# Optimization experiments

Measured on AMD Instinct MI355X. Metric: run time of the kernel, lower is better.

## Reference

```python
import jax, jax.numpy as jnp
import numpy as np

B, S, D = 16, 4096, 1024
DIM_K, DIM_V, NUM_HEAD = 1024, 1024, 16


def setup_inputs() -> dict:
    key = jax.random.key(0)
    ks = jax.random.split(key, 7)
    s_in = 1.0 / np.sqrt(D)
    return {
        "x": jax.random.normal(ks[0], (B, S, D), dtype=jnp.float32),
        "Wq": jax.random.normal(ks[1], (D, DIM_K), dtype=jnp.float32) * s_in,
        "bq": jnp.zeros((DIM_K,), dtype=jnp.float32),
        "Wk": jax.random.normal(ks[2], (D, DIM_K), dtype=jnp.float32) * s_in,
        "bk": jnp.zeros((DIM_K,), dtype=jnp.float32),
        "Wv": jax.random.normal(ks[3], (D, DIM_V), dtype=jnp.float32) * s_in,
        "bv": jnp.zeros((DIM_V,), dtype=jnp.float32),
    }


def reference(x, Wq, bq, Wk, bk, Wv, bv):
    H = NUM_HEAD
    b, s, _ = x.shape
    Q = x @ Wq + bq                      # (B,S,dim_k)
    K = x @ Wk + bk                      # (B,S,dim_k)
    V = x @ Wv + bv                      # (B,S,dim_v)
    Q_ = Q.reshape(b, s, H, DIM_K // H)  # (B,S,H,dk)
    K_ = K.reshape(b, s, H, DIM_K // H)
    V_ = V.reshape(b, s, H, DIM_V // H)
    # NOTE: faithful to the source quirk — scores are across HEADS (H x H)
    # at each (batch, seq) position; no 1/sqrt(dim_k) scaling (unused in source).
    scores = jnp.einsum("bshd,bsgd->bshg", Q_, K_)   # (B,S,H,H)
    atten = jax.nn.softmax(scores, axis=-1)
    out = jnp.einsum("bshg,bsgd->bshd", atten, V_)    # (B,S,H,dv_head)
    return out.reshape(b, s, -1)                      # (B,S,dim_v)
```

## Files before the change

kernel.cpp:

```cpp
#include <hip/hip_runtime.h>
#include <stdint.h>

#define M_TOTAL 65536
#define DIM     1024
#define NQKV    3072
#define NHEAD   16
#define HDIM    64

typedef __attribute__((ext_vector_type(8))) _Float16 f16x8;
typedef __attribute__((ext_vector_type(4))) _Float16 f16x4;
typedef __attribute__((ext_vector_type(4))) float    f32x4;

__global__ __launch_bounds__(256) void cvt_x_kernel(const float* __restrict__ x,
                                                    _Float16* __restrict__ xh,
                                                    int n4) {
    int i = blockIdx.x * blockDim.x + threadIdx.x;
    int stride = gridDim.x * blockDim.x;
    const float4* x4 = (const float4*)x;
    f16x4* o4 = (f16x4*)xh;
    for (; i < n4; i += stride) {
        float4 v = x4[i];
        f16x4 o;
        o[0] = (_Float16)v.x; o[1] = (_Float16)v.y;
        o[2] = (_Float16)v.z; o[3] = (_Float16)v.w;
        o4[i] = o;
    }
}

__global__ void cvt_w_kernel(const float* __restrict__ Wq,
                             const float* __restrict__ Wk,
                             const float* __restrict__ Wv,
                             _Float16* __restrict__ Wt) {
    __shared__ float tile[32][33];
    int which = blockIdx.z;
    const float* W = (which == 0) ? Wq : (which == 1) ? Wk : Wv;
    int d0 = blockIdx.y * 32, n0 = blockIdx.x * 32;
    int tx = threadIdx.x, ty = threadIdx.y;
    tile[ty][tx] = W[(size_t)(d0 + ty) * DIM + n0 + tx];
    __syncthreads();
    Wt[(size_t)(which * DIM + n0 + ty) * DIM + d0 + tx] = (_Float16)tile[tx][ty];
}

__global__ __launch_bounds__(256) void bias_kernel(const float* __restrict__ bq,
                                                   const float* __restrict__ bk,
                                                   const float* __restrict__ bv,
                                                   float* __restrict__ bias) {
    int i = blockIdx.x * 256 + threadIdx.x;
    if (i < NQKV)
        bias[i] = (i < 1024) ? bq[i] : (i < 2048) ? bk[i - 1024] : bv[i - 2048];
}


#define LDSA(slot)  ((slot) << 15)
#define LDSB(slot)  (65536 + ((slot) << 15))

#define MFMA_Q(MIBASE, NIBASE)                                                  \
    __builtin_amdgcn_s_setprio(1);                                              \
    _Pragma("unroll") for (int mi = 0; mi < 4; ++mi)                            \
    _Pragma("unroll") for (int ni = 0; ni < 2; ++ni)                            \
    _Pragma("unroll") for (int ks = 0; ks < 2; ++ks)                            \
        acc[(MIBASE) + mi][(NIBASE) + ni] = __builtin_amdgcn_mfma_f32_16x16x32_f16( \
            b[(NIBASE) + ni][ks], a[mi][ks], acc[(MIBASE) + mi][(NIBASE) + ni], 0, 0, 0); \
    __builtin_amdgcn_s_setprio(0);

__global__ __launch_bounds__(512, 2) void qkv_gemm_kernel(const _Float16* __restrict__ Xh,
                                                          const _Float16* __restrict__ Wth,
                                                          const float* __restrict__ bias,
                                                          _Float16* __restrict__ Ch) {
    extern __shared__ char smem[];

    const int bid = blockIdx.x;
    const int swz = (bid & 7) * (3072 / 8) + (bid >> 3);
    const int tm  = swz / (NQKV / 256);
    const int tn  = swz % (NQKV / 256);
    const int brow = tm * 256;
    const int bcol = tn * 256;

    const int tid = threadIdx.x;
    const int w   = tid >> 6;
    const int l   = tid & 63;
    const int wm  = w >> 2;
    const int wn  = w & 3;

    const int lrow8 = l >> 3;
    const int lcol8 = (l & 7) ^ lrow8;
    const _Float16* pAsrc = Xh  + (size_t)(brow + w * 8 + lrow8) * DIM + lcol8 * 8;
    const _Float16* pBsrc = Wth + (size_t)(bcol + w * 8 + lrow8) * DIM + lcol8 * 8;

    auto stA = [&](int slot, int kt, int half) {
        const _Float16* s = pAsrc + ((size_t)half << 17) + ((size_t)kt << 6);
        char* d = smem + LDSA(slot) + (half << 14) + (w << 10);
        __builtin_amdgcn_global_load_lds((const __attribute__((address_space(1))) void*)s,
                                         (__attribute__((address_space(3))) void*)d, 16, 0, 0);
        __builtin_amdgcn_global_load_lds((const __attribute__((address_space(1))) void*)(s + (1 << 16)),
                                         (__attribute__((address_space(3))) void*)(d + 8192), 16, 0, 0);
    };
    auto stB = [&](int slot, int kt, int half) {
        const _Float16* s = pBsrc + ((size_t)half << 17) + ((size_t)kt << 6);
        char* d = smem + LDSB(slot) + (half << 14) + (w << 10);
        __builtin_amdgcn_global_load_lds((const __attribute__((address_space(1))) void*)s,
                                         (__attribute__((address_space(3))) void*)d, 16, 0, 0);
        __builtin_amdgcn_global_load_lds((const __attribute__((address_space(1))) void*)(s + (1 << 16)),
                                         (__attribute__((address_space(3))) void*)(d + 8192), 16, 0, 0);
    };

    const int aRowB = ((wm << 7) + (l & 15)) << 7;
    const int bRowB = 65536 + (((wn << 6) + (l & 15)) << 7);
    const int xk0 = (((l >> 4) ^ (l & 7)) << 4);
    const int xk1 = ((((l >> 4) + 4) ^ (l & 7)) << 4);
    auto LDA = [&](int slot, int mi, int ks) -> f16x8 {
        return *(const f16x8*)(smem + (slot << 15) + aRowB + (mi << 11) + (ks ? xk1 : xk0));
    };
    auto LDB = [&](int slot, int ni, int ks) -> f16x8 {
        return *(const f16x8*)(smem + (slot << 15) + bRowB + (ni << 11) + (ks ? xk1 : xk0));
    };

    f32x4 acc[8][4] = {};
    f16x8 a[4][2], b[4][2];

    stB(0, 0, 0); stB(0, 0, 1);
    stA(0, 0, 0); stA(0, 0, 1);
    stB(1, 1, 0); stB(1, 1, 1);
    asm volatile("s_waitcnt vmcnt(2)" ::: "memory");
    __builtin_amdgcn_s_barrier();
    __builtin_amdgcn_sched_barrier(0);

#pragma unroll 1
    for (int i = 0; i < 7; ++i) {
        const int u = 2 * i;
#pragma unroll
        for (int mi = 0; mi < 4; ++mi) { a[mi][0] = LDA(0, mi, 0); a[mi][1] = LDA(0, mi, 1); }
#pragma unroll
        for (int ni = 0; ni < 2; ++ni) { b[ni][0] = LDB(0, ni, 0); b[ni][1] = LDB(0, ni, 1); }
        stA(1, u + 1, 0);
        __builtin_amdgcn_s_barrier();
        MFMA_Q(0, 0)
        __builtin_amdgcn_s_barrier();
        b[2][0] = LDB(0, 2, 0); b[2][1] = LDB(0, 2, 1);
        b[3][0] = LDB(0, 3, 0); b[3][1] = LDB(0, 3, 1);
        stA(1, u + 1, 1);
        __builtin_amdgcn_s_barrier();
        MFMA_Q(0, 2)
        __builtin_amdgcn_s_barrier();
#pragma unroll
        for (int mi = 0; mi < 4; ++mi) { a[mi][0] = LDA(0, mi + 4, 0); a[mi][1] = LDA(0, mi + 4, 1); }
        stB(0, u + 2, 0);
        __builtin_amdgcn_s_barrier();
        MFMA_Q(4, 0)
        __builtin_amdgcn_s_barrier();
        stB(0, u + 2, 1);
        asm volatile("s_waitcnt vmcnt(4)" ::: "memory");
        __builtin_amdgcn_s_barrier();
        __builtin_amdgcn_sched_barrier(0);
        MFMA_Q(4, 2)
        __builtin_amdgcn_s_barrier();
#pragma unroll
        for (int mi = 0; mi < 4; ++mi) { a[mi][0] = LDA(1, mi, 0); a[mi][1] = LDA(1, mi, 1); }
#pragma unroll
        for (int ni = 0; ni < 2; ++ni) { b[ni][0] = LDB(1, ni, 0); b[ni][1] = LDB(1, ni, 1); }
        stA(0, u + 2, 0);
        __builtin_amdgcn_s_barrier();
        MFMA_Q(0, 0)
        __builtin_amdgcn_s_barrier();
        b[2][0] = LDB(1, 2, 0); b[2][1] = LDB(1, 2, 1);
        b[3][0] = LDB(1, 3, 0); b[3][1] = LDB(1, 3, 1);
        stA(0, u + 2, 1);
        __builtin_amdgcn_s_barrier();
        MFMA_Q(0, 2)
        __builtin_amdgcn_s_barrier();
#pragma unroll
        for (int mi = 0; mi < 4; ++mi) { a[mi][0] = LDA(1, mi + 4, 0); a[mi][1] = LDA(1, mi + 4, 1); }
        stB(1, u + 3, 0);
        __builtin_amdgcn_s_barrier();
        MFMA_Q(4, 0)
        __builtin_amdgcn_s_barrier();
        stB(1, u + 3, 1);
        asm volatile("s_waitcnt vmcnt(4)" ::: "memory");
        __builtin_amdgcn_s_barrier();
        __builtin_amdgcn_sched_barrier(0);
        MFMA_Q(4, 2)
        __builtin_amdgcn_s_barrier();
    }

    {
#pragma unroll
        for (int mi = 0; mi < 4; ++mi) { a[mi][0] = LDA(0, mi, 0); a[mi][1] = LDA(0, mi, 1); }
#pragma unroll
        for (int ni = 0; ni < 2; ++ni) { b[ni][0] = LDB(0, ni, 0); b[ni][1] = LDB(0, ni, 1); }
        stA(1, 15, 0);
        __builtin_amdgcn_s_barrier();
        MFMA_Q(0, 0)
        __builtin_amdgcn_s_barrier();
        b[2][0] = LDB(0, 2, 0); b[2][1] = LDB(0, 2, 1);
        b[3][0] = LDB(0, 3, 0); b[3][1] = LDB(0, 3, 1);
        stA(1, 15, 1);
        __builtin_amdgcn_s_barrier();
        MFMA_Q(0, 2)
        __builtin_amdgcn_s_barrier();
#pragma unroll
        for (int mi = 0; mi < 4; ++mi) { a[mi][0] = LDA(0, mi + 4, 0); a[mi][1] = LDA(0, mi + 4, 1); }
        __builtin_amdgcn_s_barrier();
        MFMA_Q(4, 0)
        __builtin_amdgcn_s_barrier();
        asm volatile("s_waitcnt vmcnt(0)" ::: "memory");
        __builtin_amdgcn_s_barrier();
        __builtin_amdgcn_sched_barrier(0);
        MFMA_Q(4, 2)
        __builtin_amdgcn_s_barrier();
#pragma unroll
        for (int mi = 0; mi < 4; ++mi) { a[mi][0] = LDA(1, mi, 0); a[mi][1] = LDA(1, mi, 1); }
#pragma unroll
        for (int ni = 0; ni < 2; ++ni) { b[ni][0] = LDB(1, ni, 0); b[ni][1] = LDB(1, ni, 1); }
        __builtin_amdgcn_s_barrier();
        MFMA_Q(0, 0)
        __builtin_amdgcn_s_barrier();
        b[2][0] = LDB(1, 2, 0); b[2][1] = LDB(1, 2, 1);
        b[3][0] = LDB(1, 3, 0); b[3][1] = LDB(1, 3, 1);
        __builtin_amdgcn_s_barrier();
        MFMA_Q(0, 2)
        __builtin_amdgcn_s_barrier();
#pragma unroll
        for (int mi = 0; mi < 4; ++mi) { a[mi][0] = LDA(1, mi + 4, 0); a[mi][1] = LDA(1, mi + 4, 1); }
        __builtin_amdgcn_s_barrier();
        MFMA_Q(4, 0)
        MFMA_Q(4, 2)
    }

    __syncthreads();
#pragma unroll
    for (int mi = 0; mi < 8; ++mi) {
        const int m = (wm << 7) + (mi << 4) + (l & 15);
        const int msw = m & 7;
#pragma unroll
        for (int ni = 0; ni < 4; ++ni) {
            const int n0 = (wn << 6) + (ni << 4) + ((l >> 4) << 2);
            const float4 bv4 = *(const float4*)&bias[bcol + n0];
            f16x4 h;
            h[0] = (_Float16)(acc[mi][ni][0] + bv4.x);
            h[1] = (_Float16)(acc[mi][ni][1] + bv4.y);
            h[2] = (_Float16)(acc[mi][ni][2] + bv4.z);
            h[3] = (_Float16)(acc[mi][ni][3] + bv4.w);
            const int c8 = n0 >> 2;
            *(f16x4*)(smem + m * 512 + (((c8 >> 1) ^ msw) << 4) + ((c8 & 1) << 3)) = h;
        }
    }
    __syncthreads();
#pragma unroll
    for (int it = 0; it < 16; ++it) {
        const int row = (tid >> 5) + (it << 4);
        const int c16 = tid & 31;
        f16x8 vv = *(const f16x8*)(smem + row * 512 + ((c16 ^ (row & 7)) << 4));
        *(f16x8*)&Ch[(size_t)(brow + row) * NQKV + bcol + (c16 << 3)] = vv;
    }
}

__global__ __launch_bounds__(256) void attn_kernel(const _Float16* __restrict__ QKVh,
                                                   float* __restrict__ out) {
    __shared__ _Float16 vlds[4][1024];
    __shared__ float attlds[4][16][16];

    const int w = threadIdx.x >> 6, l = threadIdx.x & 63;
    const size_t p = (size_t)blockIdx.x * 4 + w;
    const _Float16* base = QKVh + p * NQKV;
    const _Float16* qrow = base;
    const _Float16* krow = base + 1024;
    const _Float16* vrow = base + 2048;
    const int h = l & 15;
    const int g4 = (l >> 4) * 4;

    *(uint4*)&vlds[w][l * 16]     = *(const uint4*)&vrow[l * 16];
    *(uint4*)&vlds[w][l * 16 + 8] = *(const uint4*)&vrow[l * 16 + 8];

    const int fo = (l & 15) * HDIM + (l >> 4) * 8;
    f16x8 aK0 = *(const f16x8*)&krow[fo];
    f16x8 aK1 = *(const f16x8*)&krow[fo + 32];
    f16x8 bQ0 = *(const f16x8*)&qrow[fo];
    f16x8 bQ1 = *(const f16x8*)&qrow[fo + 32];

    f32x4 sT = {0.f, 0.f, 0.f, 0.f};
    sT = __builtin_amdgcn_mfma_f32_16x16x32_f16(aK0, bQ0, sT, 0, 0, 0);
    sT = __builtin_amdgcn_mfma_f32_16x16x32_f16(aK1, bQ1, sT, 0, 0, 0);

    float m = fmaxf(fmaxf(sT[0], sT[1]), fmaxf(sT[2], sT[3]));
    m = fmaxf(m, __shfl_xor(m, 16));
    m = fmaxf(m, __shfl_xor(m, 32));
    float e0 = __expf(sT[0] - m), e1 = __expf(sT[1] - m);
    float e2 = __expf(sT[2] - m), e3 = __expf(sT[3] - m);
    float s = e0 + e1 + e2 + e3;
    s += __shfl_xor(s, 16);
    s += __shfl_xor(s, 32);
    const float inv = 1.0f / s;

    float4 att = make_float4(e0 * inv, e1 * inv, e2 * inv, e3 * inv);
    *(float4*)&attlds[w][h][g4] = att;
    __syncthreads();

    const int dbase = (l >> 4) * 16;
    float acc[16];
#pragma unroll
    for (int c = 0; c < 16; ++c) acc[c] = 0.f;

#pragma unroll
    for (int g = 0; g < 16; ++g) {
        const float av = attlds[w][h][g];
        f16x8 v0 = *(const f16x8*)&vlds[w][g * HDIM + dbase];
        f16x8 v1 = *(const f16x8*)&vlds[w][g * HDIM + dbase + 8];
#pragma unroll
        for (int c = 0; c < 8; ++c) {
            acc[c]     += av * (float)v0[c];
            acc[c + 8] += av * (float)v1[c];
        }
    }

    float* op = out + p * DIM + h * HDIM + dbase;
#pragma unroll
    for (int c = 0; c < 16; c += 4)
        *(float4*)(op + c) = make_float4(acc[c], acc[c + 1], acc[c + 2], acc[c + 3]);
}

extern "C" void kernel_launch(void* const* d_in, const int* in_sizes, int n_in,
                              void* d_out, int out_size, void* d_ws, size_t ws_size,
                              hipStream_t stream) {
    const float* x  = (const float*)d_in[0];
    const float* Wq = (const float*)d_in[1];
    const float* bq = (const float*)d_in[2];
    const float* Wk = (const float*)d_in[3];
    const float* bk = (const float*)d_in[4];
    const float* Wv = (const float*)d_in[5];
    const float* bv = (const float*)d_in[6];
    float* out = (float*)d_out;

    char* ws = (char*)d_ws;
    _Float16* Xh  = (_Float16*)ws;
    _Float16* Wth = (_Float16*)(ws + 134217728);
    float*    bias = (float*)(ws + 134217728 + 6291456);
    _Float16* Ch  = (_Float16*)(ws + 134217728 + 6291456 + 12288);

    (void)hipFuncSetAttribute((const void*)qkv_gemm_kernel,
                              hipFuncAttributeMaxDynamicSharedMemorySize, 131072);

    hipLaunchKernelGGL(cvt_x_kernel, dim3(2048), dim3(256), 0, stream,
                       x, Xh, (M_TOTAL * DIM) / 4);
    hipLaunchKernelGGL(cvt_w_kernel, dim3(32, 32, 3), dim3(32, 32), 0, stream,
                       Wq, Wk, Wv, Wth);
    hipLaunchKernelGGL(bias_kernel, dim3(12), dim3(256), 0, stream,
                       bq, bk, bv, bias);
    hipLaunchKernelGGL(qkv_gemm_kernel, dim3((M_TOTAL / 256) * (NQKV / 256)), dim3(512), 131072, stream,
                       Xh, Wth, bias, Ch);
    hipLaunchKernelGGL(attn_kernel, dim3(M_TOTAL / 4), dim3(256), 0, stream,
                       Ch, out);
}
```

Before: 618.6 us.

## Simplify QKV GEMM main loop to one MFMA block per k-tile

Replaces the hand-interleaved quarter-tile schedule of the QKV GEMM. That schedule used many barriers and LDS-read/MFMA phases. The new loop preloads all A and B fragments for a k-tile into registers, issues the whole 8x4 MFMA block, then stages the tile two steps ahead with one barrier pair per iteration. It aims to cut barrier and scheduling overhead. In exchange it reduces overlap of LDS reads with MFMA work and raises register pressure. It also issues redundant clamped loads of the last k-tile in the final iterations.

```diff
diff --git a/kernel.cpp b/kernel.cpp
--- a/kernel.cpp
+++ b/kernel.cpp
@@ -54,15 +54,6 @@
 #define LDSA(slot)  ((slot) << 15)
 #define LDSB(slot)  (65536 + ((slot) << 15))
 
-#define MFMA_Q(MIBASE, NIBASE)                                                  \
-    __builtin_amdgcn_s_setprio(1);                                              \
-    _Pragma("unroll") for (int mi = 0; mi < 4; ++mi)                            \
-    _Pragma("unroll") for (int ni = 0; ni < 2; ++ni)                            \
-    _Pragma("unroll") for (int ks = 0; ks < 2; ++ks)                            \
-        acc[(MIBASE) + mi][(NIBASE) + ni] = __builtin_amdgcn_mfma_f32_16x16x32_f16( \
-            b[(NIBASE) + ni][ks], a[mi][ks], acc[(MIBASE) + mi][(NIBASE) + ni], 0, 0, 0); \
-    __builtin_amdgcn_s_setprio(0);
-
 __global__ __launch_bounds__(512, 2) void qkv_gemm_kernel(const _Float16* __restrict__ Xh,
                                                           const _Float16* __restrict__ Wth,
                                                           const float* __restrict__ bias,
@@ -87,21 +78,23 @@
     const _Float16* pAsrc = Xh  + (size_t)(brow + w * 8 + lrow8) * DIM + lcol8 * 8;
     const _Float16* pBsrc = Wth + (size_t)(bcol + w * 8 + lrow8) * DIM + lcol8 * 8;
 
-    auto stA = [&](int slot, int kt, int half) {
-        const _Float16* s = pAsrc + ((size_t)half << 17) + ((size_t)kt << 6);
-        char* d = smem + LDSA(slot) + (half << 14) + (w << 10);
-        __builtin_amdgcn_global_load_lds((const __attribute__((address_space(1))) void*)s,
-                                         (__attribute__((address_space(3))) void*)d, 16, 0, 0);
-        __builtin_amdgcn_global_load_lds((const __attribute__((address_space(1))) void*)(s + (1 << 16)),
-                                         (__attribute__((address_space(3))) void*)(d + 8192), 16, 0, 0);
-    };
-    auto stB = [&](int slot, int kt, int half) {
-        const _Float16* s = pBsrc + ((size_t)half << 17) + ((size_t)kt << 6);
-        char* d = smem + LDSB(slot) + (half << 14) + (w << 10);
-        __builtin_amdgcn_global_load_lds((const __attribute__((address_space(1))) void*)s,
-                                         (__attribute__((address_space(3))) void*)d, 16, 0, 0);
-        __builtin_amdgcn_global_load_lds((const __attribute__((address_space(1))) void*)(s + (1 << 16)),
-                                         (__attribute__((address_space(3))) void*)(d + 8192), 16, 0, 0);
+    auto stageA = [&](int slot, int kt) {
+#pragma unroll
+        for (int ln = 0; ln < 4; ++ln) {
+            const _Float16* s = pAsrc + (size_t)(ln * 64) * DIM + ((size_t)kt << 6);
+            char* d = smem + LDSA(slot) + ln * 8192 + (w << 10);
+            __builtin_amdgcn_global_load_lds((const __attribute__((address_space(1))) void*)s,
+                                             (__attribute__((address_space(3))) void*)d, 16, 0, 0);
+        }
+    };
+    auto stageB = [&](int slot, int kt) {
+#pragma unroll
+        for (int ln = 0; ln < 4; ++ln) {
+            const _Float16* s = pBsrc + (size_t)(ln * 64) * DIM + ((size_t)kt << 6);
+            char* d = smem + LDSB(slot) + ln * 8192 + (w << 10);
+            __builtin_amdgcn_global_load_lds((const __attribute__((address_space(1))) void*)s,
+                                             (__attribute__((address_space(3))) void*)d, 16, 0, 0);
+        }
     };
 
     const int aRowB = ((wm << 7) + (l & 15)) << 7;
@@ -116,114 +109,50 @@
     };
 
     f32x4 acc[8][4] = {};
-    f16x8 a[4][2], b[4][2];
-
-    stB(0, 0, 0); stB(0, 0, 1);
-    stA(0, 0, 0); stA(0, 0, 1);
-    stB(1, 1, 0); stB(1, 1, 1);
-    asm volatile("s_waitcnt vmcnt(2)" ::: "memory");
+    f16x8 a[8][2], b[4][2];
+
+    auto READS = [&](int slot) {
+#pragma unroll
+        for (int mi = 0; mi < 8; ++mi) { a[mi][0] = LDA(slot, mi, 0); a[mi][1] = LDA(slot, mi, 1); }
+#pragma unroll
+        for (int ni = 0; ni < 4; ++ni) { b[ni][0] = LDB(slot, ni, 0); b[ni][1] = LDB(slot, ni, 1); }
+    };
+
+    stageA(0, 0); stageB(0, 0);
+    stageA(1, 1); stageB(1, 1);
+    asm volatile("s_waitcnt vmcnt(8)" ::: "memory");
     __builtin_amdgcn_s_barrier();
     __builtin_amdgcn_sched_barrier(0);
+    READS(0);
 
 #pragma unroll 1
-    for (int i = 0; i < 7; ++i) {
-        const int u = 2 * i;
-#pragma unroll
-        for (int mi = 0; mi < 4; ++mi) { a[mi][0] = LDA(0, mi, 0); a[mi][1] = LDA(0, mi, 1); }
-#pragma unroll
-        for (int ni = 0; ni < 2; ++ni) { b[ni][0] = LDB(0, ni, 0); b[ni][1] = LDB(0, ni, 1); }
-        stA(1, u + 1, 0);
+    for (int u = 0; u < 16; ++u) {
+        const int s = u & 1;
+
+        __builtin_amdgcn_s_setprio(1);
+#pragma unroll
+        for (int mi = 0; mi < 8; ++mi)
+#pragma unroll
+            for (int ni = 0; ni < 4; ++ni) {
+                acc[mi][ni] = __builtin_amdgcn_mfma_f32_16x16x32_f16(b[ni][0], a[mi][0], acc[mi][ni], 0, 0, 0);
+                acc[mi][ni] = __builtin_amdgcn_mfma_f32_16x16x32_f16(b[ni][1], a[mi][1], acc[mi][ni], 0, 0, 0);
+            }
+        __builtin_amdgcn_s_setprio(0);
+
+        asm volatile("s_waitcnt lgkmcnt(0)" ::: "memory");
+        __builtin_amdgcn_sched_barrier(0);
         __builtin_amdgcn_s_barrier();
-        MFMA_Q(0, 0)
+        __builtin_amdgcn_sched_barrier(0);
+
+        int kt = u + 2; if (kt > 15) kt = 15;
+        stageA(s, kt); stageB(s, kt);
+
+        asm volatile("s_waitcnt vmcnt(8)" ::: "memory");
+        __builtin_amdgcn_sched_barrier(0);
         __builtin_amdgcn_s_barrier();
-        b[2][0] = LDB(0, 2, 0); b[2][1] = LDB(0, 2, 1);
-        b[3][0] = LDB(0, 3, 0); b[3][1] = LDB(0, 3, 1);
-        stA(1, u + 1, 1);
-        __builtin_amdgcn_s_barrier();
-        MFMA_Q(0, 2)
-        __builtin_amdgcn_s_barrier();
-#pragma unroll
-        for (int mi = 0; mi < 4; ++mi) { a[mi][0] = LDA(0, mi + 4, 0); a[mi][1] = LDA(0, mi + 4, 1); }
-        stB(0, u + 2, 0);
-        __builtin_amdgcn_s_barrier();
-        MFMA_Q(4, 0)
-        __builtin_amdgcn_s_barrier();
-        stB(0, u + 2, 1);
-        asm volatile("s_waitcnt vmcnt(4)" ::: "memory");
-        __builtin_amdgcn_s_barrier();
-        __builtin_amdgcn_sched_barrier(0);
-        MFMA_Q(4, 2)
-        __builtin_amdgcn_s_barrier();
-#pragma unroll
-        for (int mi = 0; mi < 4; ++mi) { a[mi][0] = LDA(1, mi, 0); a[mi][1] = LDA(1, mi, 1); }
-#pragma unroll
-        for (int ni = 0; ni < 2; ++ni) { b[ni][0] = LDB(1, ni, 0); b[ni][1] = LDB(1, ni, 1); }
-        stA(0, u + 2, 0);
-        __builtin_amdgcn_s_barrier();
-        MFMA_Q(0, 0)
-        __builtin_amdgcn_s_barrier();
-        b[2][0] = LDB(1, 2, 0); b[2][1] = LDB(1, 2, 1);
-        b[3][0] = LDB(1, 3, 0); b[3][1] = LDB(1, 3, 1);
-        stA(0, u + 2, 1);
-        __builtin_amdgcn_s_barrier();
-        MFMA_Q(0, 2)
-        __builtin_amdgcn_s_barrier();
-#pragma unroll
-        for (int mi = 0; mi < 4; ++mi) { a[mi][0] = LDA(1, mi + 4, 0); a[mi][1] = LDA(1, mi + 4, 1); }
-        stB(1, u + 3, 0);
-        __builtin_amdgcn_s_barrier();
-        MFMA_Q(4, 0)
-        __builtin_amdgcn_s_barrier();
-        stB(1, u + 3, 1);
-        asm volatile("s_waitcnt vmcnt(4)" ::: "memory");
-        __builtin_amdgcn_s_barrier();
-        __builtin_amdgcn_sched_barrier(0);
-        MFMA_Q(4, 2)
-        __builtin_amdgcn_s_barrier();
-    }
-
-    {
-#pragma unroll
-        for (int mi = 0; mi < 4; ++mi) { a[mi][0] = LDA(0, mi, 0); a[mi][1] = LDA(0, mi, 1); }
-#pragma unroll
-        for (int ni = 0; ni < 2; ++ni) { b[ni][0] = LDB(0, ni, 0); b[ni][1] = LDB(0, ni, 1); }
-        stA(1, 15, 0);
-        __builtin_amdgcn_s_barrier();
-        MFMA_Q(0, 0)
-        __builtin_amdgcn_s_barrier();
-        b[2][0] = LDB(0, 2, 0); b[2][1] = LDB(0, 2, 1);
-        b[3][0] = LDB(0, 3, 0); b[3][1] = LDB(0, 3, 1);
-        stA(1, 15, 1);
-        __builtin_amdgcn_s_barrier();
-        MFMA_Q(0, 2)
-        __builtin_amdgcn_s_barrier();
-#pragma unroll
-        for (int mi = 0; mi < 4; ++mi) { a[mi][0] = LDA(0, mi + 4, 0); a[mi][1] = LDA(0, mi + 4, 1); }
-        __builtin_amdgcn_s_barrier();
-        MFMA_Q(4, 0)
-        __builtin_amdgcn_s_barrier();
-        asm volatile("s_waitcnt vmcnt(0)" ::: "memory");
-        __builtin_amdgcn_s_barrier();
-        __builtin_amdgcn_sched_barrier(0);
-        MFMA_Q(4, 2)
-        __builtin_amdgcn_s_barrier();
-#pragma unroll
-        for (int mi = 0; mi < 4; ++mi) { a[mi][0] = LDA(1, mi, 0); a[mi][1] = LDA(1, mi, 1); }
-#pragma unroll
-        for (int ni = 0; ni < 2; ++ni) { b[ni][0] = LDB(1, ni, 0); b[ni][1] = LDB(1, ni, 1); }
-        __builtin_amdgcn_s_barrier();
-        MFMA_Q(0, 0)
-        __builtin_amdgcn_s_barrier();
-        b[2][0] = LDB(1, 2, 0); b[2][1] = LDB(1, 2, 1);
-        b[3][0] = LDB(1, 3, 0); b[3][1] = LDB(1, 3, 1);
-        __builtin_amdgcn_s_barrier();
-        MFMA_Q(0, 2)
-        __builtin_amdgcn_s_barrier();
-#pragma unroll
-        for (int mi = 0; mi < 4; ++mi) { a[mi][0] = LDA(1, mi + 4, 0); a[mi][1] = LDA(1, mi + 4, 1); }
-        __builtin_amdgcn_s_barrier();
-        MFMA_Q(4, 0)
-        MFMA_Q(4, 2)
+        __builtin_amdgcn_sched_barrier(0);
+
+        READS(1 - s);
     }
 
     __syncthreads();
```

After: 675.7 us. 1.09x slower.

## Fuse fp32-to-fp16 conversion of x into GEMM A-tile loading

Applied to the files above, without the earlier changes.

Drops the separate cvt_x kernel and has the QKV GEMM read fp32 x straight into registers, convert it to fp16 and write it into swizzled LDS, in place of the direct global-to-LDS fp16 loads. This removes a full write and re-read of the 128 MB fp16 copy of x plus one launch. In exchange, each GEMM tile reads twice as many bytes of A, and x is re-read by all 12 column tiles. It also costs extra VGPRs for the staging buffer and extra LDS write/wait instructions inside the tightly scheduled MFMA pipeline.

```diff
diff --git a/kernel.cpp b/kernel.cpp
--- a/kernel.cpp
+++ b/kernel.cpp
@@ -10,22 +10,6 @@
 typedef __attribute__((ext_vector_type(8))) _Float16 f16x8;
 typedef __attribute__((ext_vector_type(4))) _Float16 f16x4;
 typedef __attribute__((ext_vector_type(4))) float    f32x4;
-
-__global__ __launch_bounds__(256) void cvt_x_kernel(const float* __restrict__ x,
-                                                    _Float16* __restrict__ xh,
-                                                    int n4) {
-    int i = blockIdx.x * blockDim.x + threadIdx.x;
-    int stride = gridDim.x * blockDim.x;
-    const float4* x4 = (const float4*)x;
-    f16x4* o4 = (f16x4*)xh;
-    for (; i < n4; i += stride) {
-        float4 v = x4[i];
-        f16x4 o;
-        o[0] = (_Float16)v.x; o[1] = (_Float16)v.y;
-        o[2] = (_Float16)v.z; o[3] = (_Float16)v.w;
-        o4[i] = o;
-    }
-}
 
 __global__ void cvt_w_kernel(const float* __restrict__ Wq,
                              const float* __restrict__ Wk,
@@ -63,7 +47,12 @@
             b[(NIBASE) + ni][ks], a[mi][ks], acc[(MIBASE) + mi][(NIBASE) + ni], 0, 0, 0); \
     __builtin_amdgcn_s_setprio(0);
 
-__global__ __launch_bounds__(512, 2) void qkv_gemm_kernel(const _Float16* __restrict__ Xh,
+#define LGKM0    do { asm volatile("s_waitcnt lgkmcnt(0)" ::: "memory");        \
+                      __builtin_amdgcn_sched_barrier(0); } while (0)
+#define VMCNT(n) do { asm volatile("s_waitcnt vmcnt(" #n ")" ::: "memory");     \
+                      __builtin_amdgcn_sched_barrier(0); } while (0)
+
+__global__ __launch_bounds__(512, 2) void qkv_gemm_kernel(const float* __restrict__ Xf,
                                                           const _Float16* __restrict__ Wth,
                                                           const float* __restrict__ bias,
                                                           _Float16* __restrict__ Ch) {
@@ -84,17 +73,8 @@
 
     const int lrow8 = l >> 3;
     const int lcol8 = (l & 7) ^ lrow8;
-    const _Float16* pAsrc = Xh  + (size_t)(brow + w * 8 + lrow8) * DIM + lcol8 * 8;
     const _Float16* pBsrc = Wth + (size_t)(bcol + w * 8 + lrow8) * DIM + lcol8 * 8;
 
-    auto stA = [&](int slot, int kt, int half) {
-        const _Float16* s = pAsrc + ((size_t)half << 17) + ((size_t)kt << 6);
-        char* d = smem + LDSA(slot) + (half << 14) + (w << 10);
-        __builtin_amdgcn_global_load_lds((const __attribute__((address_space(1))) void*)s,
-                                         (__attribute__((address_space(3))) void*)d, 16, 0, 0);
-        __builtin_amdgcn_global_load_lds((const __attribute__((address_space(1))) void*)(s + (1 << 16)),
-                                         (__attribute__((address_space(3))) void*)(d + 8192), 16, 0, 0);
-    };
     auto stB = [&](int slot, int kt, int half) {
         const _Float16* s = pBsrc + ((size_t)half << 17) + ((size_t)kt << 6);
         char* d = smem + LDSB(slot) + (half << 14) + (w << 10);
@@ -104,6 +84,29 @@
                                          (__attribute__((address_space(3))) void*)(d + 8192), 16, 0, 0);
     };
 
+    const int ar0 = (w << 2) + (l >> 4);
+    const int ac  = (l & 15) << 2;
+    const float* pAsrc = Xf + (size_t)(brow + ar0) * DIM + ac;
+    float4 abuf[8];
+    auto issueA = [&](int kt) {
+#pragma unroll
+        for (int j = 0; j < 8; ++j)
+            abuf[j] = *(const float4*)(pAsrc + ((size_t)(32 * j) * DIM) + (kt << 6));
+    };
+    const int ag   = ac >> 3;
+    const int ahalf = (ac >> 2) & 1;
+    const int agsw = ag ^ (ar0 & 7);
+    auto writeA = [&](int slot) {
+#pragma unroll
+        for (int j = 0; j < 8; ++j) {
+            const int r = ar0 + 32 * j;
+            f16x4 h;
+            h[0] = (_Float16)abuf[j].x; h[1] = (_Float16)abuf[j].y;
+            h[2] = (_Float16)abuf[j].z; h[3] = (_Float16)abuf[j].w;
+            *(f16x4*)(smem + LDSA(slot) + (r << 7) + (agsw << 4) + (ahalf << 3)) = h;
+        }
+    };
+
     const int aRowB = ((wm << 7) + (l & 15)) << 7;
     const int bRowB = 65536 + (((wn << 6) + (l & 15)) << 7);
     const int xk0 = (((l >> 4) ^ (l & 7)) << 4);
@@ -118,10 +121,13 @@
     f32x4 acc[8][4] = {};
     f16x8 a[4][2], b[4][2];
 
+    issueA(0);
     stB(0, 0, 0); stB(0, 0, 1);
-    stA(0, 0, 0); stA(0, 0, 1);
+    VMCNT(4);
+    writeA(0);
     stB(1, 1, 0); stB(1, 1, 1);
-    asm volatile("s_waitcnt vmcnt(2)" ::: "memory");
+    VMCNT(4);
+    LGKM0;
     __builtin_amdgcn_s_barrier();
     __builtin_amdgcn_sched_barrier(0);
 
@@ -132,13 +138,12 @@
         for (int mi = 0; mi < 4; ++mi) { a[mi][0] = LDA(0, mi, 0); a[mi][1] = LDA(0, mi, 1); }
 #pragma unroll
         for (int ni = 0; ni < 2; ++ni) { b[ni][0] = LDB(0, ni, 0); b[ni][1] = LDB(0, ni, 1); }
-        stA(1, u + 1, 0);
+        issueA(u + 1);
         __builtin_amdgcn_s_barrier();
         MFMA_Q(0, 0)
         __builtin_amdgcn_s_barrier();
         b[2][0] = LDB(0, 2, 0); b[2][1] = LDB(0, 2, 1);
         b[3][0] = LDB(0, 3, 0); b[3][1] = LDB(0, 3, 1);
-        stA(1, u + 1, 1);
         __builtin_amdgcn_s_barrier();
         MFMA_Q(0, 2)
         __builtin_amdgcn_s_barrier();
@@ -149,7 +154,9 @@
         MFMA_Q(4, 0)
         __builtin_amdgcn_s_barrier();
         stB(0, u + 2, 1);
-        asm volatile("s_waitcnt vmcnt(4)" ::: "memory");
+        VMCNT(4);
+        writeA(1);
+        LGKM0;
         __builtin_amdgcn_s_barrier();
         __builtin_amdgcn_sched_barrier(0);
         MFMA_Q(4, 2)
@@ -158,13 +165,12 @@
         for (int mi = 0; mi < 4; ++mi) { a[mi][0] = LDA(1, mi, 0); a[mi][1] = LDA(1, mi, 1); }
 #pragma unroll
         for (int ni = 0; ni < 2; ++ni) { b[ni][0] = LDB(1, ni, 0); b[ni][1] = LDB(1, ni, 1); }
-        stA(0, u + 2, 0);
+        issueA(u + 2);
         __builtin_amdgcn_s_barrier();
         MFMA_Q(0, 0)
         __builtin_amdgcn_s_barrier();
         b[2][0] = LDB(1, 2, 0); b[2][1] = LDB(1, 2, 1);
         b[3][0] = LDB(1, 3, 0); b[3][1] = LDB(1, 3, 1);
-        stA(0, u + 2, 1);
         __builtin_amdgcn_s_barrier();
         MFMA_Q(0, 2)
         __builtin_amdgcn_s_barrier();
@@ -175,7 +181,9 @@
         MFMA_Q(4, 0)
         __builtin_amdgcn_s_barrier();
         stB(1, u + 3, 1);
-        asm volatile("s_waitcnt vmcnt(4)" ::: "memory");
+        VMCNT(4);
+        writeA(0);
+        LGKM0;
         __builtin_amdgcn_s_barrier();
         __builtin_amdgcn_sched_barrier(0);
         MFMA_Q(4, 2)
@@ -187,13 +195,12 @@
         for (int mi = 0; mi < 4; ++mi) { a[mi][0] = LDA(0, mi, 0); a[mi][1] = LDA(0, mi, 1); }
 #pragma unroll
         for (int ni = 0; ni < 2; ++ni) { b[ni][0] = LDB(0, ni, 0); b[ni][1] = LDB(0, ni, 1); }
-        stA(1, 15, 0);
+        issueA(15);
         __builtin_amdgcn_s_barrier();
         MFMA_Q(0, 0)
         __builtin_amdgcn_s_barrier();
         b[2][0] = LDB(0, 2, 0); b[2][1] = LDB(0, 2, 1);
         b[3][0] = LDB(0, 3, 0); b[3][1] = LDB(0, 3, 1);
-        stA(1, 15, 1);
         __builtin_amdgcn_s_barrier();
         MFMA_Q(0, 2)
         __builtin_amdgcn_s_barrier();
@@ -202,7 +209,9 @@
         __builtin_amdgcn_s_barrier();
         MFMA_Q(4, 0)
         __builtin_amdgcn_s_barrier();
-        asm volatile("s_waitcnt vmcnt(0)" ::: "memory");
+        VMCNT(0);
+        writeA(1);
+        LGKM0;
         __builtin_amdgcn_s_barrier();
         __builtin_amdgcn_sched_barrier(0);
         MFMA_Q(4, 2)
@@ -331,22 +340,19 @@
     float* out = (float*)d_out;
 
     char* ws = (char*)d_ws;
-    _Float16* Xh  = (_Float16*)ws;
-    _Float16* Wth = (_Float16*)(ws + 134217728);
-    float*    bias = (float*)(ws + 134217728 + 6291456);
-    _Float16* Ch  = (_Float16*)(ws + 134217728 + 6291456 + 12288);
+    _Float16* Wth  = (_Float16*)ws;
+    float*    bias = (float*)(ws + 6291456);
+    _Float16* Ch   = (_Float16*)(ws + 6291456 + 12288);
 
     (void)hipFuncSetAttribute((const void*)qkv_gemm_kernel,
                               hipFuncAttributeMaxDynamicSharedMemorySize, 131072);
 
-    hipLaunchKernelGGL(cvt_x_kernel, dim3(2048), dim3(256), 0, stream,
-                       x, Xh, (M_TOTAL * DIM) / 4);
     hipLaunchKernelGGL(cvt_w_kernel, dim3(32, 32, 3), dim3(32, 32), 0, stream,
                        Wq, Wk, Wv, Wth);
     hipLaunchKernelGGL(bias_kernel, dim3(12), dim3(256), 0, stream,
                        bq, bk, bv, bias);
     hipLaunchKernelGGL(qkv_gemm_kernel, dim3((M_TOTAL / 256) * (NQKV / 256)), dim3(512), 131072, stream,
-                       Xh, Wth, bias, Ch);
+                       x, Wth, bias, Ch);
     hipLaunchKernelGGL(attn_kernel, dim3(M_TOTAL / 4), dim3(256), 0, stream,
                        Ch, out);
 }
```

After: 744.7 us. 1.2x slower.
